# Kernel optimization log

Measured on AMD Instinct MI355X. Metric: run time of the kernel, lower is better.

The kernel has to match this reference:

```python
import jax, jax.numpy as jnp
import numpy as np

NUM_NODES = 100000
EMBED_DIM = 64
HIDDEN_DIM = 64
HEADS = 4
NEG_SLOPE = 0.2


def setup_inputs() -> dict:
    key = jax.random.key(0)
    ks = jax.random.split(key, 10)
    E = 1000000
    edge_index = jax.random.randint(ks[0], (2, E), 0, NUM_NODES, dtype=jnp.int64)
    out1 = HIDDEN_DIM // HEADS  # 16
    s = 1.0 / np.sqrt(EMBED_DIM)
    emb = jax.random.normal(ks[1], (NUM_NODES, EMBED_DIM), jnp.float32) * s
    # Layer 1: GATConv(64 -> 16, heads=4, concat=True)
    W1 = jax.random.normal(ks[2], (EMBED_DIM, HEADS * out1), jnp.float32) * s
    a_src1 = jax.random.normal(ks[3], (HEADS, out1), jnp.float32) * 0.1
    a_dst1 = jax.random.normal(ks[4], (HEADS, out1), jnp.float32) * 0.1
    b1 = jnp.zeros((HEADS * out1,), jnp.float32)
    # Layer 2: GATConv(64 -> 64, heads=1, concat=False)
    W2 = jax.random.normal(ks[5], (HIDDEN_DIM, HIDDEN_DIM), jnp.float32) * s
    a_src2 = jax.random.normal(ks[6], (1, HIDDEN_DIM), jnp.float32) * 0.1
    a_dst2 = jax.random.normal(ks[7], (1, HIDDEN_DIM), jnp.float32) * 0.1
    b2 = jnp.zeros((HIDDEN_DIM,), jnp.float32)
    return {"edge_index": edge_index, "emb": emb,
            "W1": W1, "a_src1": a_src1, "a_dst1": a_dst1, "b1": b1,
            "W2": W2, "a_src2": a_src2, "a_dst2": a_dst2, "b2": b2}


def _gat_conv(x, src, dst, num_nodes, W, a_s, a_d, heads, out_ch):
    # x: [N, F_in]; messages flow src -> dst, softmax over incoming edges of dst.
    h = (x @ W).reshape(-1, heads, out_ch)            # [N, H, C]
    alpha_s = (h * a_s[None]).sum(-1)                 # [N, H]
    alpha_d = (h * a_d[None]).sum(-1)                 # [N, H]
    e = alpha_s[src] + alpha_d[dst]                   # [E, H]
    e = jnp.where(e > 0, e, NEG_SLOPE * e)            # LeakyReLU(0.2)
    m = jax.ops.segment_max(e, dst, num_segments=num_nodes)   # [N, H]
    w = jnp.exp(e - m[dst])                           # [E, H]
    denom = jax.ops.segment_sum(w, dst, num_segments=num_nodes)
    alpha = w / (denom[dst] + 1e-16)                  # [E, H]
    out = jax.ops.segment_sum(alpha[:, :, None] * h[src], dst,
                              num_segments=num_nodes)  # [N, H, C]
    return out


def _forward(edge_index, emb, W1, a_src1, a_dst1, b1, W2, a_src2, a_dst2, b2):
    N = emb.shape[0]
    loops = jnp.arange(N, dtype=edge_index.dtype)
    src = jnp.concatenate([edge_index[0], loops])  # PyG add_self_loops=True
    dst = jnp.concatenate([edge_index[1], loops])
    # Layer 1: heads=4, concat
    x = _gat_conv(emb, src, dst, N, W1, a_src1, a_dst1, HEADS, HIDDEN_DIM // HEADS)
    x = x.reshape(N, -1) + b1                      # concat heads -> [N, 64]
    x = jax.nn.elu(x)
    # Layer 2: heads=1, concat=False (mean over the single head)
    x = _gat_conv(x, src, dst, N, W2, a_src2, a_dst2, 1, HIDDEN_DIM)
    x = x[:, 0, :] + b2                            # [N, 64]
    # F.normalize(p=2, dim=1) with eps=1e-12
    norm = jnp.maximum(jnp.linalg.norm(x, axis=1, keepdims=True), 1e-12)
    return x / norm


def reference(edge_index, emb, W1, a_src1, a_dst1, b1, W2, a_src2, a_dst2, b2):
    return _forward(edge_index, emb, W1, a_src1, a_dst1, b1, W2, a_src2, a_dst2, b2)
```

## Files before the change

kernel.cpp:

```cpp
#include <hip/hip_runtime.h>
#include <hip/hip_fp16.h>
#include <math.h>


constexpr int FDIM = 64;
constexpr int BSHIFT = 9;
constexpr int BMASK = (1 << BSHIFT) - 1;
constexpr int EDGE_TILE = 4096;
constexpr int SLAB_CAP = 8192;

using f16 = _Float16;
typedef f16 f16x8 __attribute__((ext_vector_type(8)));
typedef f16 f16x4 __attribute__((ext_vector_type(4)));
typedef float f32x4 __attribute__((ext_vector_type(4)));


__global__ void zero_kernel(int* __restrict__ p, int n) {
  int i = blockIdx.x * blockDim.x + threadIdx.x;
  if (i < n) p[i] = 0;
}


__global__ __launch_bounds__(256) void tile_scatter_direct_kernel(
    const int* __restrict__ ei, int E, int Etot, int NB,
    int* __restrict__ bcnt, unsigned* __restrict__ slab) {
  __shared__ int hist[512];
  __shared__ int cur[512];
  int t = threadIdx.x;
  for (int b = t; b < NB; b += 256) hist[b] = 0;
  __syncthreads();
  int i0 = blockIdx.x * EDGE_TILE;
  int iend = min(i0 + EDGE_TILE, Etot);
  for (int i = i0 + t; i < iend; i += 256) {
    int dst = (i < E) ? ei[E + i] : (i - E);
    atomicAdd(&hist[dst >> BSHIFT], 1);
  }
  __syncthreads();
  for (int b = t; b < NB; b += 256)
    cur[b] = hist[b] ? atomicAdd(&bcnt[b], hist[b]) : 0;
  __syncthreads();
  for (int i = i0 + t; i < iend; i += 256) {
    int src, dst;
    if (i < E) { src = ei[i]; dst = ei[E + i]; }
    else       { src = i - E; dst = i - E; }
    int b = dst >> BSHIFT;
    int pos = atomicAdd(&cur[b], 1);
    if (pos < SLAB_CAP)
      slab[(size_t)b * SLAB_CAP + pos] =
          ((unsigned)src << BSHIFT) | (unsigned)(dst & BMASK);
  }
}

__global__ __launch_bounds__(256) void bucket_csr_kernel(
    const unsigned* __restrict__ slab, const int* __restrict__ bcnt,
    int N, int NB, int Etot,
    int* __restrict__ row_start, int* __restrict__ esrc) {
  __shared__ int hist[512];
  __shared__ int excl[512];
  __shared__ int cur[512];
  __shared__ int sbase;
  int b = blockIdx.x;
  int t = threadIdx.x;

  if (t < 64) {
    int ssum = 0;
    for (int i = t; i < b; i += 64) ssum += bcnt[i];
#pragma unroll
    for (int off = 32; off > 0; off >>= 1) ssum += __shfl_xor(ssum, off, 64);
    if (t == 0) sbase = ssum;
  }
  hist[t] = 0;
  hist[256 + t] = 0;
  __syncthreads();
  int base = sbase;
  int cnt = min(bcnt[b], SLAB_CAP);
  const unsigned* sp = slab + (size_t)b * SLAB_CAP;
  for (int i = t; i < cnt; i += 256)
    atomicAdd(&hist[sp[i] & (unsigned)BMASK], 1);
  __syncthreads();
  int h0 = hist[2 * t], h1 = hist[2 * t + 1];
  int s = h0 + h1;
  int lane = t & 63, w = t >> 6;
  int x = s;
#pragma unroll
  for (int off = 1; off < 64; off <<= 1) {
    int u = __shfl_up(x, off, 64);
    if (lane >= off) x += u;
  }
  __shared__ int wsum[4];
  if (lane == 63) wsum[w] = x;
  __syncthreads();
  int add = 0;
#pragma unroll
  for (int k = 0; k < 4; ++k) add += (k < w) ? wsum[k] : 0;
  int e0 = x + add - s;
  excl[2 * t] = e0;
  excl[2 * t + 1] = e0 + h0;
  cur[2 * t] = e0;
  cur[2 * t + 1] = e0 + h0;
  __syncthreads();
  int node0 = b << BSHIFT;
#pragma unroll
  for (int k = 0; k < 2; ++k) {
    int slot = k * 256 + t;
    int node = node0 + slot;
    if (node < N) row_start[node] = base + excl[slot];
  }
  if (b == NB - 1 && t == 0) row_start[N] = Etot;
  for (int i = t; i < cnt; i += 256) {
    unsigned p = sp[i];
    int pos = base + atomicAdd(&cur[p & (unsigned)BMASK], 1);
    esrc[pos] = (int)(p >> BSHIFT);
  }
}


template <int HEADS, typename IN>
__global__ __launch_bounds__(256) void mfma_gemm_kernel(
    const IN* __restrict__ X, const float* __restrict__ W,
    const float* __restrict__ a_s, const float* __restrict__ a_d, int N,
    __half* __restrict__ H, float* __restrict__ AS, float* __restrict__ AD,
    int nRowTiles) {
  __shared__ f16 Xs[64 * 72];
  __shared__ f16 Wt[64 * 72];
  int t = threadIdx.x;

#pragma unroll
  for (int i = 0; i < 16; ++i) {
    int idx = i * 256 + t;
    int k = idx >> 6, c = idx & 63;
    Wt[c * 72 + k] = (f16)W[idx];
  }

  int lane = t & 63, wid = t >> 6;
  int m0 = wid * 16;
  int li = lane & 15, lk = lane >> 4;
  int ko = lk * 8;
  float asc[4], adc[4];
#pragma unroll
  for (int q = 0; q < 4; ++q) {
    asc[q] = a_s[q * 16 + li];
    adc[q] = a_d[q * 16 + li];
  }

  for (int tile = blockIdx.x; tile < nRowTiles; tile += gridDim.x) {
    int row0 = tile * 64;
    __syncthreads();
    if constexpr (sizeof(IN) == 4) {
#pragma unroll
      for (int i = 0; i < 4; ++i) {
        int idx = (i * 256 + t) * 4;
        int r = idx >> 6, k = idx & 63;
        int rg = min(row0 + r, N - 1);
        float4 f = *reinterpret_cast<const float4*>(
            reinterpret_cast<const float*>(X) + (size_t)rg * 64 + k);
        f16x4 v = {(f16)f.x, (f16)f.y, (f16)f.z, (f16)f.w};
        *reinterpret_cast<f16x4*>(&Xs[r * 72 + k]) = v;
      }
    } else {
#pragma unroll
      for (int i = 0; i < 2; ++i) {
        int idx = (i * 256 + t) * 8;
        int r = idx >> 6, k = idx & 63;
        int rg = min(row0 + r, N - 1);
        f16x8 v = *reinterpret_cast<const f16x8*>(
            reinterpret_cast<const f16*>(X) + (size_t)rg * 64 + k);
        *reinterpret_cast<f16x8*>(&Xs[r * 72 + k]) = v;
      }
    }
    __syncthreads();

    f16x8 a_lo = *reinterpret_cast<const f16x8*>(&Xs[(m0 + li) * 72 + ko]);
    f16x8 a_hi = *reinterpret_cast<const f16x8*>(&Xs[(m0 + li) * 72 + 32 + ko]);

    f32x4 acc[4];
#pragma unroll
    for (int q = 0; q < 4; ++q) acc[q] = (f32x4){0.f, 0.f, 0.f, 0.f};
#pragma unroll
    for (int q = 0; q < 4; ++q) {
      int c0 = q * 16 + li;
      f16x8 b_lo = *reinterpret_cast<const f16x8*>(&Wt[c0 * 72 + ko]);
      f16x8 b_hi = *reinterpret_cast<const f16x8*>(&Wt[c0 * 72 + 32 + ko]);
      acc[q] = __builtin_amdgcn_mfma_f32_16x16x32_f16(a_lo, b_lo, acc[q], 0, 0, 0);
      acc[q] = __builtin_amdgcn_mfma_f32_16x16x32_f16(a_hi, b_hi, acc[q], 0, 0, 0);
    }

    int rbase = row0 + m0 + lk * 4;
#pragma unroll
    for (int r = 0; r < 4; ++r) {
      int grow = rbase + r;
      if (grow < N) {
#pragma unroll
        for (int q = 0; q < 4; ++q)
          H[(size_t)grow * 64 + q * 16 + li] = __float2half((float)acc[q][r]);
      }
    }

    if constexpr (HEADS == 4) {
      float ps[4][4], pd[4][4];
#pragma unroll
      for (int q = 0; q < 4; ++q)
#pragma unroll
        for (int r = 0; r < 4; ++r) {
          ps[q][r] = (float)acc[q][r] * asc[q];
          pd[q][r] = (float)acc[q][r] * adc[q];
        }
#pragma unroll
      for (int off = 1; off < 16; off <<= 1)
#pragma unroll
        for (int q = 0; q < 4; ++q)
#pragma unroll
          for (int r = 0; r < 4; ++r) {
            ps[q][r] += __shfl_xor(ps[q][r], off, 64);
            pd[q][r] += __shfl_xor(pd[q][r], off, 64);
          }
      if (li == 0) {
#pragma unroll
        for (int r = 0; r < 4; ++r) {
          int grow = rbase + r;
          if (grow < N) {
#pragma unroll
            for (int q = 0; q < 4; ++q) {
              AS[(size_t)grow * 4 + q] = ps[q][r];
              AD[(size_t)grow * 4 + q] = pd[q][r];
            }
          }
        }
      }
    } else {
      float ps[4], pd[4];
#pragma unroll
      for (int r = 0; r < 4; ++r) {
        ps[r] = 0.f; pd[r] = 0.f;
#pragma unroll
        for (int q = 0; q < 4; ++q) {
          ps[r] = fmaf((float)acc[q][r], asc[q], ps[r]);
          pd[r] = fmaf((float)acc[q][r], adc[q], pd[r]);
        }
      }
#pragma unroll
      for (int off = 1; off < 16; off <<= 1)
#pragma unroll
        for (int r = 0; r < 4; ++r) {
          ps[r] += __shfl_xor(ps[r], off, 64);
          pd[r] += __shfl_xor(pd[r], off, 64);
        }
      if (li == 0) {
#pragma unroll
        for (int r = 0; r < 4; ++r) {
          int grow = rbase + r;
          if (grow < N) { AS[grow] = ps[r]; AD[grow] = pd[r]; }
        }
      }
    }
  }
}


template <int HEADS, bool FINAL, typename OUTT>
__global__ __launch_bounds__(256) void aggregate_kernel(
    const int* __restrict__ row_start, const int* __restrict__ esrc,
    const __half* __restrict__ H, const float* __restrict__ AS,
    const float* __restrict__ AD, const float* __restrict__ bias, int N,
    OUTT* __restrict__ OUT) {
  int t = threadIdx.x;
  int wid = t >> 6;
  int half = (t >> 5) & 1;
  int ll = t & 31;
  int c = ll & 7;
  int eo = ll >> 3;
  int n = blockIdx.x * 8 + wid * 2 + half;

  int head = (HEADS == 4) ? (c >> 1) : 0;

  int rs = 0, re = 0;
  float ad = 0.f;
  if (n < N) {
    rs = row_start[n];
    re = row_start[n + 1];
    ad = AD[(size_t)n * HEADS + head];
  }
  int deg = re - rs;
  int degO = __shfl_xor(deg, 32, 64);
  int degmax = max(deg, degO);

  const f16* Hp = reinterpret_cast<const f16*>(H);

  float d = 0.f;
  float a[8] = {0.f, 0.f, 0.f, 0.f, 0.f, 0.f, 0.f, 0.f};

  for (int i = 0; i < degmax; i += 16) {
    int sv[4];
    float ev[4];
    f16x8 hv[4];
#pragma unroll
    for (int k = 0; k < 4; ++k) {
      int o = i + 4 * k + eo;
      int oc = max(min(o, deg - 1), 0);
      sv[k] = esrc[rs + oc];
    }
#pragma unroll
    for (int k = 0; k < 4; ++k) {
      ev[k] = AS[(unsigned)sv[k] * HEADS + (unsigned)head];
      hv[k] = *reinterpret_cast<const f16x8*>(&Hp[(size_t)sv[k] * 64 + c * 8]);
    }
#pragma unroll
    for (int k = 0; k < 4; ++k) {
      int o = i + 4 * k + eo;
      float e = ev[k] + ad;
      e = fmaxf(e, 0.2f * e);
      float w = (o < deg) ? __expf(e) : 0.f;
      d += w;
#pragma unroll
      for (int j = 0; j < 8; ++j) a[j] = fmaf(w, (float)hv[k][j], a[j]);
    }
  }

  d += __shfl_xor(d, 8, 64);
  d += __shfl_xor(d, 16, 64);
#pragma unroll
  for (int j = 0; j < 8; ++j) {
    a[j] += __shfl_xor(a[j], 8, 64);
    a[j] += __shfl_xor(a[j], 16, 64);
  }

  if (n >= N) return;

  float inv = 1.f / (d + 1e-16f);
  float4 b0 = reinterpret_cast<const float4*>(bias)[c * 2];
  float4 b1 = reinterpret_cast<const float4*>(bias)[c * 2 + 1];
  float v[8];
  v[0] = a[0] * inv + b0.x;
  v[1] = a[1] * inv + b0.y;
  v[2] = a[2] * inv + b0.z;
  v[3] = a[3] * inv + b0.w;
  v[4] = a[4] * inv + b1.x;
  v[5] = a[5] * inv + b1.y;
  v[6] = a[6] * inv + b1.z;
  v[7] = a[7] * inv + b1.w;

  if constexpr (FINAL) {
    float ss = 0.f;
#pragma unroll
    for (int j = 0; j < 8; ++j) ss += v[j] * v[j];
    ss += __shfl_xor(ss, 1, 64);
    ss += __shfl_xor(ss, 2, 64);
    ss += __shfl_xor(ss, 4, 64);
    float rn = 1.f / fmaxf(sqrtf(ss), 1e-12f);
    if (eo == 0) {
      float4* O4 = reinterpret_cast<float4*>(OUT);
      O4[(size_t)n * 16 + c * 2] =
          make_float4(v[0] * rn, v[1] * rn, v[2] * rn, v[3] * rn);
      O4[(size_t)n * 16 + c * 2 + 1] =
          make_float4(v[4] * rn, v[5] * rn, v[6] * rn, v[7] * rn);
    }
  } else {
#pragma unroll
    for (int j = 0; j < 8; ++j) v[j] = v[j] > 0.f ? v[j] : expm1f(v[j]);
    if (eo == 0) {
      f16x8 o = {(f16)v[0], (f16)v[1], (f16)v[2], (f16)v[3],
                 (f16)v[4], (f16)v[5], (f16)v[6], (f16)v[7]};
      reinterpret_cast<f16x8*>(OUT)[(size_t)n * 8 + c] = o;
    }
  }
}


extern "C" void kernel_launch(void* const* d_in, const int* in_sizes, int n_in,
                              void* d_out, int out_size, void* d_ws,
                              size_t ws_size, hipStream_t stream) {
  const int* ei = (const int*)d_in[0];
  const float* emb = (const float*)d_in[1];
  const float* W1 = (const float*)d_in[2];
  const float* as1 = (const float*)d_in[3];
  const float* ad1 = (const float*)d_in[4];
  const float* b1 = (const float*)d_in[5];
  const float* W2 = (const float*)d_in[6];
  const float* as2 = (const float*)d_in[7];
  const float* ad2 = (const float*)d_in[8];
  const float* b2 = (const float*)d_in[9];
  float* out = (float*)d_out;

  int E = in_sizes[0] / 2;
  int N = in_sizes[1] / FDIM;
  int Etot = E + N;
  int NB = (N + BMASK) >> BSHIFT;
  int nTiles = (Etot + EDGE_TILE - 1) / EDGE_TILE;

  char* ws = (char*)d_ws;
  size_t off = 0;
  auto alloc = [&](size_t bytes) -> void* {
    void* p = ws + off;
    off += (bytes + 255) & ~(size_t)255;
    return p;
  };
  int* bcnt = (int*)alloc((size_t)NB * sizeof(int));
  unsigned* slab = (unsigned*)alloc((size_t)NB * SLAB_CAP * sizeof(unsigned));
  int* row_start = (int*)alloc((size_t)(N + 1) * sizeof(int));
  int* esrc = (int*)alloc((size_t)Etot * sizeof(int));
  __half* hbuf = (__half*)alloc((size_t)N * FDIM * sizeof(__half));
  __half* xbuf = (__half*)alloc((size_t)N * FDIM * sizeof(__half));
  float* AS = (float*)alloc((size_t)N * 4 * sizeof(float));
  float* AD = (float*)alloc((size_t)N * 4 * sizeof(float));

  zero_kernel<<<(NB + 255) / 256, 256, 0, stream>>>(bcnt, NB);
  tile_scatter_direct_kernel<<<nTiles, 256, 0, stream>>>(ei, E, Etot, NB,
                                                         bcnt, slab);
  bucket_csr_kernel<<<NB, 256, 0, stream>>>(slab, bcnt, N, NB, Etot,
                                            row_start, esrc);

  int nRowTiles = (N + 63) / 64;
  int gmg = min(nRowTiles, 512);
  int ga = (N + 7) / 8;
  mfma_gemm_kernel<4, float><<<gmg, 256, 0, stream>>>(emb, W1, as1, ad1, N, hbuf, AS, AD, nRowTiles);
  aggregate_kernel<4, false, __half><<<ga, 256, 0, stream>>>(row_start, esrc, hbuf, AS, AD, b1, N, xbuf);
  mfma_gemm_kernel<1, __half><<<gmg, 256, 0, stream>>>(xbuf, W2, as2, ad2, N, hbuf, AS, AD, nRowTiles);
  aggregate_kernel<1, true, float><<<ga, 256, 0, stream>>>(row_start, esrc, hbuf, AS, AD, b2, N, out);
}
```

Before: 131.2 us.

## Fuse edge scatter and bucket CSR build into one kernel with grid barrier

Merges the tile-scatter kernel and the per-bucket CSR kernel into a single launch. Blocks first process edge tiles in a grid-stride loop, then meet at a global atomic spin barrier before the first NB blocks build the CSR rows. This removes one kernel launch and the gap between the two phases. In exchange it relies on all blocks being resident at once for the barrier to finish; otherwise it could deadlock. It also adds spin-polling traffic on a shared counter.

```diff
diff --git a/kernel.cpp b/kernel.cpp
--- a/kernel.cpp
+++ b/kernel.cpp
@@ -21,46 +21,52 @@
 }
 
 
-__global__ __launch_bounds__(256) void tile_scatter_direct_kernel(
-    const int* __restrict__ ei, int E, int Etot, int NB,
-    int* __restrict__ bcnt, unsigned* __restrict__ slab) {
-  __shared__ int hist[512];
-  __shared__ int cur[512];
-  int t = threadIdx.x;
-  for (int b = t; b < NB; b += 256) hist[b] = 0;
-  __syncthreads();
-  int i0 = blockIdx.x * EDGE_TILE;
-  int iend = min(i0 + EDGE_TILE, Etot);
-  for (int i = i0 + t; i < iend; i += 256) {
-    int dst = (i < E) ? ei[E + i] : (i - E);
-    atomicAdd(&hist[dst >> BSHIFT], 1);
-  }
-  __syncthreads();
-  for (int b = t; b < NB; b += 256)
-    cur[b] = hist[b] ? atomicAdd(&bcnt[b], hist[b]) : 0;
-  __syncthreads();
-  for (int i = i0 + t; i < iend; i += 256) {
-    int src, dst;
-    if (i < E) { src = ei[i]; dst = ei[E + i]; }
-    else       { src = i - E; dst = i - E; }
-    int b = dst >> BSHIFT;
-    int pos = atomicAdd(&cur[b], 1);
-    if (pos < SLAB_CAP)
-      slab[(size_t)b * SLAB_CAP + pos] =
-          ((unsigned)src << BSHIFT) | (unsigned)(dst & BMASK);
-  }
-}
-
-__global__ __launch_bounds__(256) void bucket_csr_kernel(
-    const unsigned* __restrict__ slab, const int* __restrict__ bcnt,
-    int N, int NB, int Etot,
-    int* __restrict__ row_start, int* __restrict__ esrc) {
+__global__ __launch_bounds__(256) void fused_csr_kernel(
+    const int* __restrict__ ei, int E, int Etot, int NB, int nTiles,
+    int* __restrict__ bcnt, unsigned* __restrict__ slab,
+    int N, int* __restrict__ row_start, int* __restrict__ esrc,
+    int* __restrict__ sync) {
   __shared__ int hist[512];
   __shared__ int excl[512];
   __shared__ int cur[512];
   __shared__ int sbase;
+  int t = threadIdx.x;
+
+  for (int tile = blockIdx.x; tile < nTiles; tile += gridDim.x) {
+    for (int b = t; b < NB; b += 256) hist[b] = 0;
+    __syncthreads();
+    int i0 = tile * EDGE_TILE;
+    int iend = min(i0 + EDGE_TILE, Etot);
+    for (int i = i0 + t; i < iend; i += 256) {
+      int dst = (i < E) ? ei[E + i] : (i - E);
+      atomicAdd(&hist[dst >> BSHIFT], 1);
+    }
+    __syncthreads();
+    for (int b = t; b < NB; b += 256)
+      cur[b] = hist[b] ? atomicAdd(&bcnt[b], hist[b]) : 0;
+    __syncthreads();
+    for (int i = i0 + t; i < iend; i += 256) {
+      int src, dst;
+      if (i < E) { src = ei[i]; dst = ei[E + i]; }
+      else       { src = i - E; dst = i - E; }
+      int b = dst >> BSHIFT;
+      int pos = atomicAdd(&cur[b], 1);
+      if (pos < SLAB_CAP)
+        slab[(size_t)b * SLAB_CAP + pos] =
+            ((unsigned)src << BSHIFT) | (unsigned)(dst & BMASK);
+    }
+    __syncthreads();
+  }
+
+  __threadfence();
+  if (t == 0) atomicAdd(sync, 1);
   int b = blockIdx.x;
-  int t = threadIdx.x;
+  if (b >= NB) return;
+  if (t == 0) {
+    while (atomicAdd(sync, 0) < (int)gridDim.x) { }
+  }
+  __syncthreads();
+  __threadfence();
 
   if (t < 64) {
     int ssum = 0;
@@ -394,7 +400,8 @@
     off += (bytes + 255) & ~(size_t)255;
     return p;
   };
-  int* bcnt = (int*)alloc((size_t)NB * sizeof(int));
+  int* bcnt = (int*)alloc((size_t)(NB + 1) * sizeof(int));
+  int* syncc = bcnt + NB;
   unsigned* slab = (unsigned*)alloc((size_t)NB * SLAB_CAP * sizeof(unsigned));
   int* row_start = (int*)alloc((size_t)(N + 1) * sizeof(int));
   int* esrc = (int*)alloc((size_t)Etot * sizeof(int));
@@ -403,11 +410,11 @@
   float* AS = (float*)alloc((size_t)N * 4 * sizeof(float));
   float* AD = (float*)alloc((size_t)N * 4 * sizeof(float));
 
-  zero_kernel<<<(NB + 255) / 256, 256, 0, stream>>>(bcnt, NB);
-  tile_scatter_direct_kernel<<<nTiles, 256, 0, stream>>>(ei, E, Etot, NB,
-                                                         bcnt, slab);
-  bucket_csr_kernel<<<NB, 256, 0, stream>>>(slab, bcnt, N, NB, Etot,
-                                            row_start, esrc);
+  zero_kernel<<<1, 256, 0, stream>>>(bcnt, NB + 1);
+  int gcsr = nTiles;
+  fused_csr_kernel<<<gcsr, 256, 0, stream>>>(ei, E, Etot, NB, nTiles,
+                                             bcnt, slab, N, row_start, esrc,
+                                             syncc);
 
   int nRowTiles = (N + 63) / 64;
   int gmg = min(nRowTiles, 512);
```

Measured after the change: 190.5 us. 45.3% more time.
